# Performance work log

Measured on AMD Instinct MI355X. Metric: run time of the kernel, lower is better.

The kernel has to match this reference:

```python
import jax, jax.numpy as jnp
import numpy as np

B, D_IN, D_H, D_OUT, D_INT = 1024, 2048, 4096, 2048, 1024


def fwht(x):
    """Fast Walsh-Hadamard transform over a length-2^k vector (unnormalized),
    faithful to the torch chunk/cat butterfly loop."""
    n = x.shape[0]
    k = int(n).bit_length() - 1
    for i in range(k):
        y = x.reshape(2 ** i, 2, -1)        # split butterfly level i
        x = jnp.stack([y[:, 0] + y[:, 1], y[:, 0] - y[:, 1]], axis=1)
    return x.reshape(n)


def fastfood(V, BB, Pi, GG, DD):
    """fastfood_torched: pad -> B*x -> H -> permute -> G* -> H -> slice/scale."""
    LL = BB.shape[0]
    vpad = jnp.zeros((LL,), V.dtype).at[: V.shape[0]].set(V)
    m5 = fwht(fwht(BB * vpad)[Pi] * GG)
    divisor = jnp.sqrt(LL * jnp.sum(GG * GG))
    return m5[:DD] / (divisor * np.sqrt(float(DD) / LL))


def _ff_vars(key, DD):
    LL = 1 << int(np.ceil(np.log2(DD)))
    k1, k2, k3 = jax.random.split(key, 3)
    BB = jnp.where(jax.random.uniform(k1, (LL,)) < 0.5, -1.0, 1.0).astype(jnp.float32)
    Pi = jax.random.permutation(k2, LL).astype(jnp.int32)
    GG = jax.random.normal(k3, (LL,), dtype=jnp.float32)
    return BB, Pi, GG


def setup_inputs():
    key = jax.random.key(0)
    ks = jax.random.split(key, 8)
    x = jax.random.normal(ks[0], (B, D_IN), dtype=jnp.float32)
    V = jax.random.normal(ks[1], (D_INT,), dtype=jnp.float32) * 0.01
    W1_0 = jax.random.normal(ks[2], (D_H, D_IN), dtype=jnp.float32) * 0.02
    b1_0 = jnp.zeros((D_H,), jnp.float32)
    W2_0 = jax.random.normal(ks[3], (D_OUT, D_H), dtype=jnp.float32) * 0.02
    b2_0 = jnp.zeros((D_OUT,), jnp.float32)
    BB_W1, Pi_W1, GG_W1 = _ff_vars(ks[4], D_H * D_IN)
    BB_b1, Pi_b1, GG_b1 = _ff_vars(ks[5], D_H)
    BB_W2, Pi_W2, GG_W2 = _ff_vars(ks[6], D_OUT * D_H)
    BB_b2, Pi_b2, GG_b2 = _ff_vars(ks[7], D_OUT)
    return dict(x=x, V=V, W1_0=W1_0, b1_0=b1_0, W2_0=W2_0, b2_0=b2_0,
                BB_W1=BB_W1, Pi_W1=Pi_W1, GG_W1=GG_W1,
                BB_b1=BB_b1, Pi_b1=Pi_b1, GG_b1=GG_b1,
                BB_W2=BB_W2, Pi_W2=Pi_W2, GG_W2=GG_W2,
                BB_b2=BB_b2, Pi_b2=Pi_b2, GG_b2=GG_b2)


def reference(x, V, W1_0, b1_0, W2_0, b2_0,
              BB_W1, Pi_W1, GG_W1, BB_b1, Pi_b1, GG_b1,
              BB_W2, Pi_W2, GG_W2, BB_b2, Pi_b2, GG_b2):
    # Reconstruct each parameter: theta = theta0 + fastfood(V).view(shape)
    W1 = W1_0 + fastfood(V, BB_W1, Pi_W1, GG_W1, D_H * D_IN).reshape(D_H, D_IN)
    b1 = b1_0 + fastfood(V, BB_b1, Pi_b1, GG_b1, D_H)
    W2 = W2_0 + fastfood(V, BB_W2, Pi_W2, GG_W2, D_OUT * D_H).reshape(D_OUT, D_H)
    b2 = b2_0 + fastfood(V, BB_b2, Pi_b2, GG_b2, D_OUT)
    # Wrapped module forward (2-layer MLP)
    h = jax.nn.relu(x @ W1.T + b1)
    return h @ W2.T + b2
```

## Files before the change

kernel.cpp:

```cpp
#include <hip/hip_runtime.h>
#include <hip/hip_bf16.h>
#include <stdint.h>


typedef __attribute__((ext_vector_type(8))) short bf16x8;
typedef __attribute__((ext_vector_type(8))) short short8;
typedef __attribute__((ext_vector_type(4))) float f32x4;

__device__ __forceinline__ ushort f2bf(float f) {
  union { float f; uint32_t u; } v; v.f = f;
  return (ushort)((v.u + 0x7FFFu + ((v.u >> 16) & 1u)) >> 16);
}
__device__ __forceinline__ float bf2f(ushort u) {
  union { uint32_t u; float f; } v; v.u = (uint32_t)u << 16; return v.f;
}

__device__ __forceinline__ void gload_lds16(const void* g, void* l) {
  __builtin_amdgcn_global_load_lds(
      (const __attribute__((address_space(1))) void*)g,
      (__attribute__((address_space(3))) void*)l, 16, 0, 0);
}

__device__ __forceinline__ void wait_vm16() { asm volatile("s_waitcnt vmcnt(16)" ::: "memory"); }
__device__ __forceinline__ void wait_vm8()  { asm volatile("s_waitcnt vmcnt(8)"  ::: "memory"); }
__device__ __forceinline__ void wait_vm0()  { asm volatile("s_waitcnt vmcnt(0)"  ::: "memory"); }
__device__ __forceinline__ void wait_lgkm0(){ asm volatile("s_waitcnt lgkmcnt(0)" ::: "memory"); }
__device__ __forceinline__ void barrier_raw(){ asm volatile("s_barrier" ::: "memory"); }

template <int NN>
__device__ __forceinline__ void wht_inreg(float* v) {
#pragma unroll
  for (int h = 1; h < NN; h <<= 1)
#pragma unroll
    for (int g = 0; g < NN; g += (h << 1))
#pragma unroll
      for (int k = 0; k < h; ++k) {
        float a = v[g + k], b = v[g + k + h];
        v[g + k] = a + b; v[g + k + h] = a - b;
      }
}

__global__ __launch_bounds__(256) void make_t_kernel(
    const float* __restrict__ V, const float* __restrict__ BB1,
    const float* __restrict__ BB2, float* __restrict__ t1, float* __restrict__ t2) {
  __shared__ float ts[1024];
  const float* BB = blockIdx.x ? BB2 : BB1;
  float* t = blockIdx.x ? t2 : t1;
  int tid = threadIdx.x;
  for (int i = tid; i < 1024; i += 256) ts[i] = BB[i] * V[i];
  for (int st = 0; st < 10; ++st) {
    int half = 1 << st;
    __syncthreads();
    for (int j = tid; j < 512; j += 256) {
      int p = ((j >> st) << (st + 1)) | (j & (half - 1));
      float a = ts[p], b = ts[p + half];
      ts[p] = a + b; ts[p + half] = a - b;
    }
  }
  __syncthreads();
  for (int i = tid; i < 1024; i += 256) t[i] = ts[i];
}

__global__ __launch_bounds__(256) void make_bias_kernel(
    const float* __restrict__ V,
    const float* __restrict__ BB1, const int* __restrict__ Pi1, const float* __restrict__ GG1, const float* __restrict__ b10,
    const float* __restrict__ BB2, const int* __restrict__ Pi2, const float* __restrict__ GG2, const float* __restrict__ b20,
    float* __restrict__ ob1, float* __restrict__ ob2) {
  __shared__ float ts[1024];
  __shared__ float zs[4096];
  __shared__ float red[4];
  int tid = threadIdx.x;
  int which = blockIdx.x;
  int L = which ? 2048 : 4096;
  const float* BB = which ? BB2 : BB1;
  const int* Pi = which ? Pi2 : Pi1;
  const float* GG = which ? GG2 : GG1;
  const float* b0 = which ? b20 : b10;
  float* ob = which ? ob2 : ob1;

  for (int i = tid; i < 1024; i += 256) ts[i] = BB[i] * V[i];
  for (int st = 0; st < 10; ++st) {
    int half = 1 << st;
    __syncthreads();
    for (int j = tid; j < 512; j += 256) {
      int p = ((j >> st) << (st + 1)) | (j & (half - 1));
      float a = ts[p], b = ts[p + half];
      ts[p] = a + b; ts[p + half] = a - b;
    }
  }
  __syncthreads();
  float gsum = 0.f;
  for (int i = tid; i < L; i += 256) {
    int pi = Pi[i];
    float g = GG[i];
    gsum += g * g;
    zs[i] = ts[pi & 1023] * g;
  }
  for (int o = 32; o > 0; o >>= 1) gsum += __shfl_down(gsum, o);
  if ((tid & 63) == 0) red[tid >> 6] = gsum;
  __syncthreads();
  float ssum = red[0] + red[1] + red[2] + red[3];
  for (int st = 0; (1 << st) < L; ++st) {
    int half = 1 << st;
    __syncthreads();
    for (int j = tid; j < (L >> 1); j += 256) {
      int p = ((j >> st) << (st + 1)) | (j & (half - 1));
      float a = zs[p], b = zs[p + half];
      zs[p] = a + b; zs[p + half] = a - b;
    }
  }
  __syncthreads();
  float scale = rsqrtf((float)L * ssum);
  for (int i = tid; i < L; i += 256) ob[i] = b0[i] + zs[i] * scale;
}

__global__ __launch_bounds__(512) void ff_pass1(
    const int* __restrict__ Pi1, const float* __restrict__ GG1,
    const int* __restrict__ Pi2, const float* __restrict__ GG2,
    const float* __restrict__ t1, const float* __restrict__ t2,
    ushort* __restrict__ inter1, ushort* __restrict__ inter2,
    float* __restrict__ partials) {
  __shared__ float ts[1024];
  __shared__ ushort zs[2][8704];
  __shared__ float red[2][4];
  const int tid = threadIdx.x;
  const int half = tid >> 8;
  const int s = tid & 255;
  const int wsel = blockIdx.x >> 9;
  const int chunk = ((blockIdx.x & 511) << 1) | half;
  const int* Pi = wsel ? Pi2 : Pi1;
  const float* GG = wsel ? GG2 : GG1;
  const float* t = wsel ? t2 : t1;
  ushort* inter = wsel ? inter2 : inter1;
  const size_t base = (size_t)chunk << 13;
  ushort* zc = zs[half];

  for (int i = tid; i < 1024; i += 512) ts[i] = t[i];

  const int4* Pi4 = (const int4*)(Pi + base);
  const float4* GG4 = (const float4*)(GG + base);
  int4 p4[8]; float4 g4[8];
#pragma unroll
  for (int j = 0; j < 8; ++j) { p4[j] = Pi4[(s << 3) + j]; g4[j] = GG4[(s << 3) + j]; }
  __syncthreads();

  float v[32];
  float gsum = 0.f;
#pragma unroll
  for (int j = 0; j < 8; ++j) {
    gsum += g4[j].x * g4[j].x + g4[j].y * g4[j].y + g4[j].z * g4[j].z + g4[j].w * g4[j].w;
    v[4 * j + 0] = ts[p4[j].x & 1023] * g4[j].x;
    v[4 * j + 1] = ts[p4[j].y & 1023] * g4[j].y;
    v[4 * j + 2] = ts[p4[j].z & 1023] * g4[j].z;
    v[4 * j + 3] = ts[p4[j].w & 1023] * g4[j].w;
  }
  wht_inreg<32>(v);

  for (int o = 32; o > 0; o >>= 1) gsum += __shfl_down(gsum, o);
  if ((s & 63) == 0) red[half][s >> 6] = gsum;

#pragma unroll
  for (int j = 0; j < 16; ++j) {
    ushort2 u; u.x = f2bf(v[2 * j]); u.y = f2bf(v[2 * j + 1]);
    *(ushort2*)&zc[34 * s + 2 * j] = u;
  }
  __syncthreads();
  if (s == 0)
    partials[(wsel << 10) + chunk] = red[half][0] + red[half][1] + red[half][2] + red[half][3];

  {
    const int pb = (s & 31) + 1088 * (s >> 5);
#pragma unroll
    for (int r = 0; r < 32; ++r) v[r] = bf2f(zc[pb + 34 * r]);
    wht_inreg<32>(v);
#pragma unroll
    for (int r = 0; r < 32; ++r) zc[pb + 34 * r] = f2bf(v[r]);
  }
  __syncthreads();

  {
    const int pc = 4 * s + 2 * (s >> 3);
    float w[4][8];
#pragma unroll
    for (int r = 0; r < 8; ++r)
#pragma unroll
      for (int kk = 0; kk < 2; ++kk) {
        ushort2 u = *(const ushort2*)&zc[pc + 1088 * r + 2 * kk];
        w[2 * kk][r] = bf2f(u.x);
        w[2 * kk + 1][r] = bf2f(u.y);
      }
#pragma unroll
    for (int k = 0; k < 4; ++k) wht_inreg<8>(w[k]);
    ushort* op = inter + base + 4 * s;
#pragma unroll
    for (int r = 0; r < 8; ++r) {
      short4 o;
      o.x = (short)f2bf(w[0][r]); o.y = (short)f2bf(w[1][r]);
      o.z = (short)f2bf(w[2][r]); o.w = (short)f2bf(w[3][r]);
      *(short4*)&op[r << 10] = o;
    }
  }
}

__global__ __launch_bounds__(256) void ff_pass2a(
    ushort* __restrict__ inter1, ushort* __restrict__ inter2) {
  const int tid = threadIdx.x;
  const int wsel = blockIdx.x >> 9;
  const int bb = blockIdx.x & 511;
  const int g0 = bb >> 4;
  const int cb = (bb & 15) << 9;
  ushort* inter = wsel ? inter2 : inter1;
  ushort* p = inter + ((size_t)(g0 << 5) << 13) + cb + (tid << 1);

  float va[32], vb[32];
#pragma unroll
  for (int r = 0; r < 32; ++r) {
    ushort2 u = *(const ushort2*)(p + ((size_t)r << 13));
    va[r] = bf2f(u.x); vb[r] = bf2f(u.y);
  }
  wht_inreg<32>(va);
  wht_inreg<32>(vb);
#pragma unroll
  for (int r = 0; r < 32; ++r) {
    ushort2 u; u.x = f2bf(va[r]); u.y = f2bf(vb[r]);
    *(ushort2*)(p + ((size_t)r << 13)) = u;
  }
}

__global__ __launch_bounds__(256) void ff_pass2b(
    const ushort* __restrict__ inter1, const ushort* __restrict__ inter2,
    const float* __restrict__ W01, const float* __restrict__ W02,
    const float* __restrict__ partials,
    ushort* __restrict__ W1b, ushort* __restrict__ W2b) {
  __shared__ float red[4];
  const int tid = threadIdx.x;
  const int wsel = blockIdx.x >> 9;
  const int bb = blockIdx.x & 511;
  const int g = bb >> 4;
  const int cb = (bb & 15) << 9;
  const ushort* inter = wsel ? inter2 : inter1;
  const float* W0 = wsel ? W02 : W01;
  ushort* Wb = wsel ? W2b : W1b;

  float ssum = 0.f;
#pragma unroll
  for (int j = 0; j < 4; ++j) ssum += partials[(wsel << 10) + tid + (j << 8)];
  for (int o = 32; o > 0; o >>= 1) ssum += __shfl_down(ssum, o);
  if ((tid & 63) == 0) red[tid >> 6] = ssum;
  __syncthreads();
  const float sc = rsqrtf(8388608.f * (red[0] + red[1] + red[2] + red[3]));

  const size_t coff = (size_t)cb + (tid << 1);
  const ushort* p = inter + ((size_t)g << 13) + coff;

  float va[32], vb[32];
#pragma unroll
  for (int r = 0; r < 32; ++r) {
    ushort2 u = *(const ushort2*)(p + ((size_t)(r << 5) << 13));
    va[r] = bf2f(u.x); vb[r] = bf2f(u.y);
  }
  wht_inreg<32>(va);
  wht_inreg<32>(vb);
#pragma unroll
  for (int r = 0; r < 32; ++r) {
    size_t m = (((size_t)(g + (r << 5))) << 13) + coff;
    float2 w0 = *(const float2*)(W0 + m);
    ushort2 u;
    u.x = f2bf(va[r] * sc + w0.x);
    u.y = f2bf(vb[r] * sc + w0.y);
    *(ushort2*)(Wb + m) = u;
  }
}

__global__ __launch_bounds__(256) void cvt_f32_bf16(
    const float4* __restrict__ in, ushort4* __restrict__ out, int n4) {
  int i = blockIdx.x * 256 + threadIdx.x;
  if (i < n4) {
    float4 v = in[i];
    ushort4 o;
    o.x = f2bf(v.x); o.y = f2bf(v.y); o.z = f2bf(v.z); o.w = f2bf(v.w);
    out[i] = o;
  }
}

template <int EPI, int NT>
__global__ __launch_bounds__(256) void gemm_bt(
    const ushort* __restrict__ A, const ushort* __restrict__ B,
    const float* __restrict__ bias, ushort* __restrict__ Cb, float* __restrict__ Cf,
    int M, int N, int K) {
  __shared__ ushort As[4][8192];
  __shared__ ushort Bs[4][8192];
  const int tid = threadIdx.x;
  const int w = tid >> 6, l = tid & 63;
  const int wr = w >> 1, wc = w & 1;
  const int brow = blockIdx.y << 7, bcol = blockIdx.x << 7;
  const int lrow = l >> 3;
  const int csrc = ((l & 7) ^ lrow) << 3;
  const int l15 = l & 15;
  const int x7 = l15 & 7;
  const int kb = blockIdx.z * (NT << 6);
  f32x4 acc[4][4] = {};

  const ushort* pa = A + (size_t)(brow + (w << 5) + lrow) * K + kb + csrc;
  const ushort* pb = B + (size_t)(bcol + (w << 5) + lrow) * K + kb + csrc;
  const size_t K8 = (size_t)K << 3;

#define STAGE(buf, tt)                                                      \
  {                                                                         \
    const ushort* qa = pa + ((tt) << 6);                                    \
    const ushort* qb = pb + ((tt) << 6);                                    \
    _Pragma("unroll")                                                       \
    for (int i = 0; i < 4; ++i) {                                           \
      gload_lds16(qa + K8 * i, &As[buf][(((w << 2) + i) << 9)]);            \
      gload_lds16(qb + K8 * i, &Bs[buf][(((w << 2) + i) << 9)]);            \
    }                                                                       \
  }

  STAGE(0, 0); STAGE(1, 1); STAGE(2, 2);
  for (int t = 0; t < NT; ++t) {
    if (t < NT - 2) wait_vm16();
    else if (t == NT - 2) wait_vm8();
    else wait_vm0();
    barrier_raw();
    if (t + 3 < NT) STAGE((t + 3) & 3, t + 3);
    const ushort* Acur = As[t & 3];
    const ushort* Bcur = Bs[t & 3];
    bf16x8 af[2][4], bfr[2][4];
#pragma unroll
    for (int kk = 0; kk < 2; ++kk) {
      int c8 = (kk << 2) + (l >> 4);
#pragma unroll
      for (int m = 0; m < 4; ++m)
        af[kk][m] = *(const bf16x8*)&Acur[(((wr << 6) + (m << 4) + l15) << 6) + ((c8 ^ x7) << 3)];
#pragma unroll
      for (int n = 0; n < 4; ++n)
        bfr[kk][n] = *(const bf16x8*)&Bcur[(((wc << 6) + (n << 4) + l15) << 6) + ((c8 ^ x7) << 3)];
    }
    wait_lgkm0();
#pragma unroll
    for (int kk = 0; kk < 2; ++kk)
#pragma unroll
      for (int m = 0; m < 4; ++m)
#pragma unroll
        for (int n = 0; n < 4; ++n)
          acc[m][n] = __builtin_amdgcn_mfma_f32_16x16x32_bf16(af[kk][m], bfr[kk][n], acc[m][n], 0, 0, 0);
  }
#undef STAGE

  if (EPI == 0) {
#pragma unroll
    for (int n = 0; n < 4; ++n) {
      int col = bcol + (wc << 6) + (n << 4) + l15;
      float bv = bias[col];
#pragma unroll
      for (int m = 0; m < 4; ++m) {
        int row0 = brow + (wr << 6) + (m << 4) + ((l >> 4) << 2);
#pragma unroll
        for (int j = 0; j < 4; ++j) {
          float vv = fmaxf(acc[m][n][j] + bv, 0.f);
          Cb[(size_t)(row0 + j) * N + col] = f2bf(vv);
        }
      }
    }
  } else {
    float* outp = Cf + (size_t)blockIdx.z * M * N;
#pragma unroll
    for (int n = 0; n < 4; ++n) {
      int col = bcol + (wc << 6) + (n << 4) + l15;
#pragma unroll
      for (int m = 0; m < 4; ++m) {
        int row0 = brow + (wr << 6) + (m << 4) + ((l >> 4) << 2);
#pragma unroll
        for (int j = 0; j < 4; ++j)
          outp[(size_t)(row0 + j) * N + col] = acc[m][n][j];
      }
    }
  }
}

__global__ __launch_bounds__(256) void reduce_out(
    const float4* __restrict__ P, const float* __restrict__ b2,
    float4* __restrict__ out) {
  int i = blockIdx.x * 256 + threadIdx.x;
  float4 a = P[i], b = P[i + 524288];
  const float4 bb = *(const float4*)(b2 + ((i & 511) << 2));
  float4 o;
  o.x = a.x + b.x + bb.x; o.y = a.y + b.y + bb.y;
  o.z = a.z + b.z + bb.z; o.w = a.w + b.w + bb.w;
  out[i] = o;
}

extern "C" void kernel_launch(void* const* d_in, const int* in_sizes, int n_in,
                              void* d_out, int out_size, void* d_ws, size_t ws_size,
                              hipStream_t stream) {
  const float* x     = (const float*)d_in[0];
  const float* V     = (const float*)d_in[1];
  const float* W1_0  = (const float*)d_in[2];
  const float* b1_0  = (const float*)d_in[3];
  const float* W2_0  = (const float*)d_in[4];
  const float* b2_0  = (const float*)d_in[5];
  const float* BB_W1 = (const float*)d_in[6];
  const int*   Pi_W1 = (const int*)d_in[7];
  const float* GG_W1 = (const float*)d_in[8];
  const float* BB_b1 = (const float*)d_in[9];
  const int*   Pi_b1 = (const int*)d_in[10];
  const float* GG_b1 = (const float*)d_in[11];
  const float* BB_W2 = (const float*)d_in[12];
  const int*   Pi_W2 = (const int*)d_in[13];
  const float* GG_W2 = (const float*)d_in[14];
  const float* BB_b2 = (const float*)d_in[15];
  const int*   Pi_b2 = (const int*)d_in[16];
  const float* GG_b2 = (const float*)d_in[17];
  float* out = (float*)d_out;

  const size_t MB = 1048576ull;
  char* ws = (char*)d_ws;
  ushort* inter1 = (ushort*)(ws);
  float*  P      = (float*)(ws);
  ushort* inter2 = (ushort*)(ws + 16 * MB);
  ushort* W1b    = (ushort*)(ws + 32 * MB);
  ushort* W2b    = (ushort*)(ws + 48 * MB);
  ushort* xb     = (ushort*)(ws + 64 * MB);
  ushort* hb     = (ushort*)(ws + 68 * MB);
  char*   S      = ws + 76 * MB;
  float*  t1     = (float*)(S);
  float*  t2     = (float*)(S + 4096);
  float*  b1     = (float*)(S + 8192);
  float*  b2     = (float*)(S + 8192 + 16384);
  float*  parts  = (float*)(S + 8192 + 16384 + 8192);

  make_t_kernel<<<2, 256, 0, stream>>>(V, BB_W1, BB_W2, t1, t2);
  make_bias_kernel<<<2, 256, 0, stream>>>(V, BB_b1, Pi_b1, GG_b1, b1_0,
                                          BB_b2, Pi_b2, GG_b2, b2_0, b1, b2);
  cvt_f32_bf16<<<2048, 256, 0, stream>>>((const float4*)x, (ushort4*)xb, 524288);

  ff_pass1<<<1024, 512, 0, stream>>>(Pi_W1, GG_W1, Pi_W2, GG_W2, t1, t2,
                                     inter1, inter2, parts);
  ff_pass2a<<<1024, 256, 0, stream>>>(inter1, inter2);
  ff_pass2b<<<1024, 256, 0, stream>>>(inter1, inter2, W1_0, W2_0, parts, W1b, W2b);

  gemm_bt<0, 32><<<dim3(32, 8, 1), 256, 0, stream>>>(xb, W1b, b1, hb, nullptr, 1024, 4096, 2048);
  gemm_bt<1, 32><<<dim3(16, 8, 2), 256, 0, stream>>>(hb, W2b, nullptr, nullptr, P, 1024, 2048, 4096);
  reduce_out<<<2048, 256, 0, stream>>>((const float4*)P, b2, (float4*)out);
}
```

Measured before the change: 181.2 us.

## Fuse FWHT pass2a/pass2b via LDS transpose and pipeline pass1 chunk loads

The two second-stage Hadamard kernels are merged into one. Each block loads a 1024x32 column slab, does the first 32-point butterfly, transposes it through LDS and does the second butterfly before adding W0, so one global round trip of the bf16 intermediate is dropped. Pass1 now runs 256 threads that each process two chunks sequentially. The second chunk's Pi/GG loads are issued before the first chunk is processed, and the LDS intermediate stays in fp32 instead of bf16. The cost is higher LDS use (fp32 zs, a 68KB tile in pass2) and lower occupancy or parallelism in both kernels.

Result: faster. 174.2 us (-3.9%).

```diff
diff --git a/kernel.cpp b/kernel.cpp
--- a/kernel.cpp
+++ b/kernel.cpp
@@ -114,160 +114,159 @@
   for (int i = tid; i < L; i += 256) ob[i] = b0[i] + zs[i] * scale;
 }
 
-__global__ __launch_bounds__(512) void ff_pass1(
+__device__ __forceinline__ void p1_load(const int* __restrict__ Pi,
+                                        const float* __restrict__ GG,
+                                        size_t base, int s, int4* p4, float4* g4) {
+  const int4* Pi4 = (const int4*)(Pi + base);
+  const float4* GG4 = (const float4*)(GG + base);
+#pragma unroll
+  for (int j = 0; j < 8; ++j) { p4[j] = Pi4[(s << 3) + j]; g4[j] = GG4[(s << 3) + j]; }
+}
+
+__device__ __forceinline__ void p1_process(
+    float* ts, float* zs, float* red, int tid, bool barA,
+    const int4* p4, const float4* g4, ushort* __restrict__ inter, size_t base,
+    float* __restrict__ partials, int chunkIdx) {
+  float v[32];
+  float gsum = 0.f;
+#pragma unroll
+  for (int j = 0; j < 8; ++j) {
+    gsum += g4[j].x * g4[j].x + g4[j].y * g4[j].y + g4[j].z * g4[j].z + g4[j].w * g4[j].w;
+    v[4 * j + 0] = ts[p4[j].x & 1023] * g4[j].x;
+    v[4 * j + 1] = ts[p4[j].y & 1023] * g4[j].y;
+    v[4 * j + 2] = ts[p4[j].z & 1023] * g4[j].z;
+    v[4 * j + 3] = ts[p4[j].w & 1023] * g4[j].w;
+  }
+  wht_inreg<32>(v);
+  for (int o = 32; o > 0; o >>= 1) gsum += __shfl_down(gsum, o);
+
+  if (barA) __syncthreads();
+  if ((tid & 63) == 0) red[tid >> 6] = gsum;
+#pragma unroll
+  for (int j = 0; j < 16; ++j) {
+    float2 u; u.x = v[2 * j]; u.y = v[2 * j + 1];
+    *(float2*)&zs[34 * tid + 2 * j] = u;
+  }
+  __syncthreads();
+  if (tid == 0) partials[chunkIdx] = red[0] + red[1] + red[2] + red[3];
+
+  {
+    const int pb = (tid & 31) + 1088 * (tid >> 5);
+#pragma unroll
+    for (int r = 0; r < 32; ++r) v[r] = zs[pb + 34 * r];
+    wht_inreg<32>(v);
+#pragma unroll
+    for (int r = 0; r < 32; ++r) zs[pb + 34 * r] = v[r];
+  }
+  __syncthreads();
+
+  {
+    const int pc = 4 * tid + 2 * (tid >> 3);
+    float w[4][8];
+#pragma unroll
+    for (int r = 0; r < 8; ++r) {
+      float2 u0 = *(const float2*)&zs[pc + 1088 * r];
+      float2 u1 = *(const float2*)&zs[pc + 1088 * r + 2];
+      w[0][r] = u0.x; w[1][r] = u0.y; w[2][r] = u1.x; w[3][r] = u1.y;
+    }
+#pragma unroll
+    for (int k = 0; k < 4; ++k) wht_inreg<8>(w[k]);
+    ushort* op = inter + base + 4 * tid;
+#pragma unroll
+    for (int r = 0; r < 8; ++r) {
+      short4 o;
+      o.x = (short)f2bf(w[0][r]); o.y = (short)f2bf(w[1][r]);
+      o.z = (short)f2bf(w[2][r]); o.w = (short)f2bf(w[3][r]);
+      *(short4*)&op[r << 10] = o;
+    }
+  }
+}
+
+__global__ __launch_bounds__(256) void ff_pass1(
     const int* __restrict__ Pi1, const float* __restrict__ GG1,
     const int* __restrict__ Pi2, const float* __restrict__ GG2,
     const float* __restrict__ t1, const float* __restrict__ t2,
     ushort* __restrict__ inter1, ushort* __restrict__ inter2,
     float* __restrict__ partials) {
   __shared__ float ts[1024];
-  __shared__ ushort zs[2][8704];
-  __shared__ float red[2][4];
+  __shared__ float zs[8704];
+  __shared__ float red[4];
   const int tid = threadIdx.x;
-  const int half = tid >> 8;
-  const int s = tid & 255;
   const int wsel = blockIdx.x >> 9;
-  const int chunk = ((blockIdx.x & 511) << 1) | half;
+  const int b = blockIdx.x & 511;
   const int* Pi = wsel ? Pi2 : Pi1;
   const float* GG = wsel ? GG2 : GG1;
   const float* t = wsel ? t2 : t1;
   ushort* inter = wsel ? inter2 : inter1;
-  const size_t base = (size_t)chunk << 13;
-  ushort* zc = zs[half];
-
-  for (int i = tid; i < 1024; i += 512) ts[i] = t[i];
-
-  const int4* Pi4 = (const int4*)(Pi + base);
-  const float4* GG4 = (const float4*)(GG + base);
-  int4 p4[8]; float4 g4[8];
-#pragma unroll
-  for (int j = 0; j < 8; ++j) { p4[j] = Pi4[(s << 3) + j]; g4[j] = GG4[(s << 3) + j]; }
-  __syncthreads();
-
-  float v[32];
-  float gsum = 0.f;
-#pragma unroll
-  for (int j = 0; j < 8; ++j) {
-    gsum += g4[j].x * g4[j].x + g4[j].y * g4[j].y + g4[j].z * g4[j].z + g4[j].w * g4[j].w;
-    v[4 * j + 0] = ts[p4[j].x & 1023] * g4[j].x;
-    v[4 * j + 1] = ts[p4[j].y & 1023] * g4[j].y;
-    v[4 * j + 2] = ts[p4[j].z & 1023] * g4[j].z;
-    v[4 * j + 3] = ts[p4[j].w & 1023] * g4[j].w;
-  }
-  wht_inreg<32>(v);
-
-  for (int o = 32; o > 0; o >>= 1) gsum += __shfl_down(gsum, o);
-  if ((s & 63) == 0) red[half][s >> 6] = gsum;
-
-#pragma unroll
-  for (int j = 0; j < 16; ++j) {
-    ushort2 u; u.x = f2bf(v[2 * j]); u.y = f2bf(v[2 * j + 1]);
-    *(ushort2*)&zc[34 * s + 2 * j] = u;
-  }
-  __syncthreads();
-  if (s == 0)
-    partials[(wsel << 10) + chunk] = red[half][0] + red[half][1] + red[half][2] + red[half][3];
-
-  {
-    const int pb = (s & 31) + 1088 * (s >> 5);
-#pragma unroll
-    for (int r = 0; r < 32; ++r) v[r] = bf2f(zc[pb + 34 * r]);
-    wht_inreg<32>(v);
-#pragma unroll
-    for (int r = 0; r < 32; ++r) zc[pb + 34 * r] = f2bf(v[r]);
-  }
-  __syncthreads();
-
-  {
-    const int pc = 4 * s + 2 * (s >> 3);
-    float w[4][8];
-#pragma unroll
-    for (int r = 0; r < 8; ++r)
-#pragma unroll
-      for (int kk = 0; kk < 2; ++kk) {
-        ushort2 u = *(const ushort2*)&zc[pc + 1088 * r + 2 * kk];
-        w[2 * kk][r] = bf2f(u.x);
-        w[2 * kk + 1][r] = bf2f(u.y);
-      }
-#pragma unroll
-    for (int k = 0; k < 4; ++k) wht_inreg<8>(w[k]);
-    ushort* op = inter + base + 4 * s;
-#pragma unroll
-    for (int r = 0; r < 8; ++r) {
-      short4 o;
-      o.x = (short)f2bf(w[0][r]); o.y = (short)f2bf(w[1][r]);
-      o.z = (short)f2bf(w[2][r]); o.w = (short)f2bf(w[3][r]);
-      *(short4*)&op[r << 10] = o;
-    }
-  }
-}
-
-__global__ __launch_bounds__(256) void ff_pass2a(
-    ushort* __restrict__ inter1, ushort* __restrict__ inter2) {
-  const int tid = threadIdx.x;
-  const int wsel = blockIdx.x >> 9;
-  const int bb = blockIdx.x & 511;
-  const int g0 = bb >> 4;
-  const int cb = (bb & 15) << 9;
-  ushort* inter = wsel ? inter2 : inter1;
-  ushort* p = inter + ((size_t)(g0 << 5) << 13) + cb + (tid << 1);
-
-  float va[32], vb[32];
-#pragma unroll
-  for (int r = 0; r < 32; ++r) {
-    ushort2 u = *(const ushort2*)(p + ((size_t)r << 13));
-    va[r] = bf2f(u.x); vb[r] = bf2f(u.y);
-  }
-  wht_inreg<32>(va);
-  wht_inreg<32>(vb);
-#pragma unroll
-  for (int r = 0; r < 32; ++r) {
-    ushort2 u; u.x = f2bf(va[r]); u.y = f2bf(vb[r]);
-    *(ushort2*)(p + ((size_t)r << 13)) = u;
-  }
-}
-
-__global__ __launch_bounds__(256) void ff_pass2b(
+  const size_t base0 = (size_t)(b * 2) << 13;
+  const size_t base1 = (size_t)(b * 2 + 1) << 13;
+  const int ci = (wsel << 10) + b * 2;
+
+  for (int i = tid; i < 1024; i += 256) ts[i] = t[i];
+  int4 pa[8]; float4 ga[8];
+  p1_load(Pi, GG, base0, tid, pa, ga);
+  __syncthreads();
+  int4 pb[8]; float4 gb[8];
+  p1_load(Pi, GG, base1, tid, pb, gb);
+  p1_process(ts, zs, red, tid, false, pa, ga, inter, base0, partials, ci);
+  p1_process(ts, zs, red, tid, true,  pb, gb, inter, base1, partials, ci + 1);
+}
+
+__global__ __launch_bounds__(512) void ff_pass2(
     const ushort* __restrict__ inter1, const ushort* __restrict__ inter2,
     const float* __restrict__ W01, const float* __restrict__ W02,
     const float* __restrict__ partials,
     ushort* __restrict__ W1b, ushort* __restrict__ W2b) {
-  __shared__ float red[4];
+  __shared__ ushort tile[1024][34];
+  __shared__ float red[8];
   const int tid = threadIdx.x;
-  const int wsel = blockIdx.x >> 9;
-  const int bb = blockIdx.x & 511;
-  const int g = bb >> 4;
-  const int cb = (bb & 15) << 9;
+  const int wsel = blockIdx.x >> 8;
+  const int cb = (blockIdx.x & 255) << 5;
   const ushort* inter = wsel ? inter2 : inter1;
   const float* W0 = wsel ? W02 : W01;
   ushort* Wb = wsel ? W2b : W1b;
 
-  float ssum = 0.f;
-#pragma unroll
-  for (int j = 0; j < 4; ++j) ssum += partials[(wsel << 10) + tid + (j << 8)];
-  for (int o = 32; o > 0; o >>= 1) ssum += __shfl_down(ssum, o);
-  if ((tid & 63) == 0) red[tid >> 6] = ssum;
-  __syncthreads();
-  const float sc = rsqrtf(8388608.f * (red[0] + red[1] + red[2] + red[3]));
-
-  const size_t coff = (size_t)cb + (tid << 1);
-  const ushort* p = inter + ((size_t)g << 13) + coff;
-
+  float s = partials[(wsel << 10) + tid] + partials[(wsel << 10) + tid + 512];
+  for (int o = 32; o > 0; o >>= 1) s += __shfl_down(s, o);
+  if ((tid & 63) == 0) red[tid >> 6] = s;
+
+  const int p = tid & 15;
+  const int g = tid >> 4;
+  const ushort* ip = inter + ((size_t)(g << 5) << 13) + cb + (p << 1);
   float va[32], vb[32];
 #pragma unroll
   for (int r = 0; r < 32; ++r) {
-    ushort2 u = *(const ushort2*)(p + ((size_t)(r << 5) << 13));
+    ushort2 u = *(const ushort2*)(ip + ((size_t)r << 13));
     va[r] = bf2f(u.x); vb[r] = bf2f(u.y);
   }
   wht_inreg<32>(va);
   wht_inreg<32>(vb);
 #pragma unroll
   for (int r = 0; r < 32; ++r) {
-    size_t m = (((size_t)(g + (r << 5))) << 13) + coff;
+    ushort2 u; u.x = f2bf(va[r]); u.y = f2bf(vb[r]);
+    *(ushort2*)&tile[(g << 5) + r][p << 1] = u;
+  }
+  __syncthreads();
+  float ssum = 0.f;
+#pragma unroll
+  for (int k = 0; k < 8; ++k) ssum += red[k];
+  const float sc = rsqrtf(8388608.f * ssum);
+
+  float wa[32], wb[32];
+#pragma unroll
+  for (int r = 0; r < 32; ++r) {
+    ushort2 u = *(const ushort2*)&tile[g + (r << 5)][p << 1];
+    wa[r] = bf2f(u.x); wb[r] = bf2f(u.y);
+  }
+  wht_inreg<32>(wa);
+  wht_inreg<32>(wb);
+#pragma unroll
+  for (int r = 0; r < 32; ++r) {
+    size_t m = (((size_t)(g + (r << 5))) << 13) + cb + (p << 1);
     float2 w0 = *(const float2*)(W0 + m);
     ushort2 u;
-    u.x = f2bf(va[r] * sc + w0.x);
-    u.y = f2bf(vb[r] * sc + w0.y);
+    u.x = f2bf(wa[r] * sc + w0.x);
+    u.y = f2bf(wb[r] * sc + w0.y);
     *(ushort2*)(Wb + m) = u;
   }
 }
@@ -434,10 +433,9 @@
                                           BB_b2, Pi_b2, GG_b2, b2_0, b1, b2);
   cvt_f32_bf16<<<2048, 256, 0, stream>>>((const float4*)x, (ushort4*)xb, 524288);
 
-  ff_pass1<<<1024, 512, 0, stream>>>(Pi_W1, GG_W1, Pi_W2, GG_W2, t1, t2,
+  ff_pass1<<<1024, 256, 0, stream>>>(Pi_W1, GG_W1, Pi_W2, GG_W2, t1, t2,
                                      inter1, inter2, parts);
-  ff_pass2a<<<1024, 256, 0, stream>>>(inter1, inter2);
-  ff_pass2b<<<1024, 256, 0, stream>>>(inter1, inter2, W1_0, W2_0, parts, W1b, W2b);
+  ff_pass2<<<512, 512, 0, stream>>>(inter1, inter2, W1_0, W2_0, parts, W1b, W2b);
 
   gemm_bt<0, 32><<<dim3(32, 8, 1), 256, 0, stream>>>(xb, W1b, b1, hb, nullptr, 1024, 4096, 2048);
   gemm_bt<1, 32><<<dim3(16, 8, 2), 256, 0, stream>>>(hb, W2b, nullptr, nullptr, P, 1024, 2048, 4096);
```
